# Kernel tuning notes

Hardware: AMD Instinct MI355X
Metric: run time of the kernel (lower is better)

Reference implementation:

```python
import jax, jax.numpy as jnp
import numpy as np

B, T, V, D, OUT = 32, 100, 10000, 128, 1000
CODE_P = 0.003  # ~30 active codes per visit


def gru_dir(x3, whh, bhh, reverse):
    """x3: [B,T,3F] precomputed input-side gates (W_ih x + b_ih). PyTorch GRU math."""
    F = whh.shape[1]
    h0 = jnp.zeros((x3.shape[0], F), x3.dtype)

    def step(h, xt):
        gh = h @ whh.T + bhh
        xr, xz, xn = jnp.split(xt, 3, -1)
        hr, hz, hn = jnp.split(gh, 3, -1)
        r = jax.nn.sigmoid(xr + hr)
        z = jax.nn.sigmoid(xz + hz)
        n = jnp.tanh(xn + r * hn)
        h_new = (1.0 - z) * n + z * h
        return h_new, h_new

    _, hs = jax.lax.scan(step, h0, jnp.swapaxes(x3, 0, 1), reverse=reverse)
    return jnp.swapaxes(hs, 0, 1)  # [B,T,F]


def setup_inputs() -> dict:
    key = jax.random.key(0)
    ks = jax.random.split(key, 16)
    s = lambda k, *sh: jax.random.normal(k, sh, dtype=jnp.float32) * 0.05
    # multi-hot visits, ~0/1 with density CODE_P; force code 0 present so no all-zero visit
    x = (jax.random.uniform(ks[0], (B, T, V)) < CODE_P).astype(jnp.float32)
    x = x.at[:, :, 0].set(1.0)
    return {
        "batchdata": x,
        "emb": s(ks[1], V, D),
        "wih_f": s(ks[2], 3 * D, D), "whh_f": s(ks[3], 3 * D, D),
        "bih_f": jnp.zeros((3 * D,), jnp.float32), "bhh_f": jnp.zeros((3 * D,), jnp.float32),
        "wih_b": s(ks[4], 3 * D, D), "whh_b": s(ks[5], 3 * D, D),
        "bih_b": jnp.zeros((3 * D,), jnp.float32), "bhh_b": jnp.zeros((3 * D,), jnp.float32),
        "attn_w": s(ks[6], 2 * D, 1), "attn_b": jnp.zeros((1,), jnp.float32),
        "comb_w": s(ks[7], D, 4 * D), "comb_b": jnp.zeros((D,), jnp.float32),
        "fc_w": s(ks[8], OUT, D), "fc_b": jnp.zeros((OUT,), jnp.float32),
    }


def reference(batchdata, emb, wih_f, whh_f, bih_f, bhh_f, wih_b, whh_b, bih_b, bhh_b,
              attn_w, attn_b, comb_w, comb_b, fc_w, fc_b):
    # multihot_to_embedding: sum of embedding rows where visit==1 == multihot @ table
    e = jnp.einsum('btv,vd->btd', batchdata, emb)          # [B,T,D]
    mask = jnp.any(e != 0, axis=2)                          # [B,T]
    # DipoleLayer: bidirectional GRU (hidden=D each dir), dropout in eval mode = identity
    xf = jnp.einsum('btf,gf->btg', e, wih_f) + bih_f
    xb = jnp.einsum('btf,gf->btg', e, wih_b) + bih_b
    hf = gru_dir(xf, whh_f, bhh_f, reverse=False)
    hb = gru_dir(xb, whh_b, bhh_b, reverse=True)
    h = jnp.concatenate([hf, hb], axis=-1)                  # [B,T,2D]
    # location-based attention over timesteps
    scores = (h @ attn_w)[..., 0] + attn_b[0]               # [B,T]
    scores = jnp.where(mask, scores, jnp.float32(-1e9))
    a = jax.nn.softmax(scores, axis=-1)
    c = jnp.einsum('bt,btf->bf', a, h)                      # [B,2D] context
    last = jnp.sum(mask.astype(jnp.int32), axis=-1) - 1     # last valid visit
    h_last = h[jnp.arange(h.shape[0]), last]                # [B,2D]
    feat = jnp.tanh(jnp.concatenate([c, h_last], -1) @ comb_w.T + comb_b)  # [B,D]
    logits = feat @ fc_w.T + fc_b                           # [B,OUT]
    return logits
```

## Files before the change

### kernel.cpp

```cpp
#include <hip/hip_runtime.h>
#include <math.h>

#define BB 32
#define TT 100
#define VV 10000
#define DD 128
#define OUTN 1000
#define G3 384

__global__ __launch_bounds__(256) void k_embed(
    const float* __restrict__ x, const float* __restrict__ emb,
    float* __restrict__ e, int* __restrict__ mask)
{
    const int bt  = blockIdx.x;
    const int tid = threadIdx.x;
    __shared__ int   s_cnt;
    __shared__ int   s_any;
    __shared__ int   s_idx[256];
    __shared__ float s_val[256];
    if (tid == 0) { s_cnt = 0; s_any = 0; }
    __syncthreads();

    const float4* x4 = (const float4*)(x + (size_t)bt * VV);
    for (int i = tid; i < VV / 4; i += 256) {
        float4 v = x4[i];
        if (v.x != 0.f) { int p = atomicAdd(&s_cnt, 1); if (p < 256) { s_idx[p] = 4*i+0; s_val[p] = v.x; } }
        if (v.y != 0.f) { int p = atomicAdd(&s_cnt, 1); if (p < 256) { s_idx[p] = 4*i+1; s_val[p] = v.y; } }
        if (v.z != 0.f) { int p = atomicAdd(&s_cnt, 1); if (p < 256) { s_idx[p] = 4*i+2; s_val[p] = v.z; } }
        if (v.w != 0.f) { int p = atomicAdd(&s_cnt, 1); if (p < 256) { s_idx[p] = 4*i+3; s_val[p] = v.w; } }
    }
    __syncthreads();
    int cnt = s_cnt; if (cnt > 256) cnt = 256;
    if (tid < DD) {
        float a0 = 0.f, a1 = 0.f, a2 = 0.f, a3 = 0.f;
        int i = 0;
        for (; i + 4 <= cnt; i += 4) {
            a0 += s_val[i+0] * emb[(size_t)s_idx[i+0] * DD + tid];
            a1 += s_val[i+1] * emb[(size_t)s_idx[i+1] * DD + tid];
            a2 += s_val[i+2] * emb[(size_t)s_idx[i+2] * DD + tid];
            a3 += s_val[i+3] * emb[(size_t)s_idx[i+3] * DD + tid];
        }
        for (; i < cnt; ++i)
            a0 += s_val[i] * emb[(size_t)s_idx[i] * DD + tid];
        float acc = (a0 + a1) + (a2 + a3);
        e[(size_t)bt * DD + tid] = acc;
        if (acc != 0.f) s_any = 1;
    }
    __syncthreads();
    if (tid == 0) mask[bt] = s_any;
}

__global__ __launch_bounds__(256) void k_gates(
    const float* __restrict__ e,
    const float* __restrict__ wih_f, const float* __restrict__ bih_f,
    const float* __restrict__ wih_b, const float* __restrict__ bih_b,
    float* __restrict__ x3)
{
    const int r0  = blockIdx.x * 8;
    const int tid = threadIdx.x;
    __shared__ __align__(16) float se[8][DD];
    for (int i = tid; i < 8 * DD; i += 256)
        se[i >> 7][i & 127] = e[(size_t)(r0 + (i >> 7)) * DD + (i & 127)];
    __syncthreads();

    const float4* wp[3];
    float bias[3];
    #pragma unroll
    for (int cc = 0; cc < 3; ++cc) {
        int col = tid + cc * 256;
        if (col < G3) { wp[cc] = (const float4*)(wih_f + (size_t)col * DD);        bias[cc] = bih_f[col]; }
        else          { wp[cc] = (const float4*)(wih_b + (size_t)(col - G3) * DD); bias[cc] = bih_b[col - G3]; }
    }

    float acc[3][8];
    #pragma unroll
    for (int cc = 0; cc < 3; ++cc)
        #pragma unroll
        for (int r = 0; r < 8; ++r) acc[cc][r] = 0.f;

    for (int k4 = 0; k4 < DD / 4; ++k4) {
        float4 ev[8];
        #pragma unroll
        for (int r = 0; r < 8; ++r) ev[r] = *(const float4*)&se[r][4 * k4];
        #pragma unroll
        for (int cc = 0; cc < 3; ++cc) {
            float4 w = wp[cc][k4];
            #pragma unroll
            for (int r = 0; r < 8; ++r)
                acc[cc][r] += ev[r].x * w.x + ev[r].y * w.y + ev[r].z * w.z + ev[r].w * w.w;
        }
    }
    #pragma unroll
    for (int cc = 0; cc < 3; ++cc) {
        int col = tid + cc * 256;
        #pragma unroll
        for (int r = 0; r < 8; ++r)
            x3[(size_t)(r0 + r) * 768 + col] = acc[cc][r] + bias[cc];
    }
}

__global__ __launch_bounds__(384, 1) void k_gru(
    const float* __restrict__ x3,
    const float* __restrict__ whh_f, const float* __restrict__ bhh_f,
    const float* __restrict__ whh_b, const float* __restrict__ bhh_b,
    float* __restrict__ h_all)
{
    const int dir = blockIdx.x & 1;
    const int b   = blockIdx.x >> 1;
    const int tid = threadIdx.x;
    const int s   = tid & 3;
    const int rg  = tid >> 2;
    const float* whh = dir ? whh_b : whh_f;
    const float* bhh = dir ? bhh_b : bhh_f;

    float4 w4[4][8];
    float  bh[4];
    #pragma unroll
    for (int j = 0; j < 4; ++j) {
        const float4* wr = (const float4*)(whh + (size_t)(rg * 4 + j) * DD + s * 32);
        #pragma unroll
        for (int k4 = 0; k4 < 8; ++k4) w4[j][k4] = wr[k4];
        bh[j] = (s == 0) ? bhh[rg * 4 + j] : 0.f;
    }

    __shared__ __align__(16) float h_pad[4 * 36];
    __shared__ float gh[G3];
    __shared__ __align__(16) float h_hist[TT * DD];

    float h_reg = 0.f;
    if (tid < 144) h_pad[tid] = 0.f;

    const int g = tid;
    const size_t xbase = (size_t)b * TT * 768 + (size_t)dir * G3;
    float xr = 0.f, xz = 0.f, xn = 0.f;
    if (tid < DD) {
        const float* xp = x3 + xbase + (size_t)(dir ? TT - 1 : 0) * 768;
        xr = xp[g]; xz = xp[DD + g]; xn = xp[2 * DD + g];
    }
    __syncthreads();

    for (int t = 0; t < TT; ++t) {
        float nxr = 0.f, nxz = 0.f, nxn = 0.f;
        if (tid < DD && t + 1 < TT) {
            const float* xp = x3 + xbase + (size_t)(dir ? TT - 2 - t : t + 1) * 768;
            nxr = xp[g]; nxz = xp[DD + g]; nxn = xp[2 * DD + g];
        }

        float a0 = bh[0], a1 = bh[1], a2 = bh[2], a3 = bh[3];
        #pragma unroll
        for (int k4 = 0; k4 < 8; ++k4) {
            float4 hv = *(const float4*)&h_pad[s * 36 + 4 * k4];
            a0 += w4[0][k4].x * hv.x + w4[0][k4].y * hv.y + w4[0][k4].z * hv.z + w4[0][k4].w * hv.w;
            a1 += w4[1][k4].x * hv.x + w4[1][k4].y * hv.y + w4[1][k4].z * hv.z + w4[1][k4].w * hv.w;
            a2 += w4[2][k4].x * hv.x + w4[2][k4].y * hv.y + w4[2][k4].z * hv.z + w4[2][k4].w * hv.w;
            a3 += w4[3][k4].x * hv.x + w4[3][k4].y * hv.y + w4[3][k4].z * hv.z + w4[3][k4].w * hv.w;
        }
        a0 += __shfl_xor(a0, 1); a1 += __shfl_xor(a1, 1);
        a2 += __shfl_xor(a2, 1); a3 += __shfl_xor(a3, 1);
        a0 += __shfl_xor(a0, 2); a1 += __shfl_xor(a1, 2);
        a2 += __shfl_xor(a2, 2); a3 += __shfl_xor(a3, 2);
        float my = (s == 0) ? a0 : (s == 1) ? a1 : (s == 2) ? a2 : a3;
        gh[tid] = my;
        __syncthreads();

        if (tid < DD) {
            float hr = gh[g], hz = gh[DD + g], hn = gh[2 * DD + g];
            float r = 1.f / (1.f + __expf(-(xr + hr)));
            float z = 1.f / (1.f + __expf(-(xz + hz)));
            float narg = xn + r * hn;
            float et = __expf(-2.f * fabsf(narg));
            float n = (1.f - et) / (1.f + et);
            n = narg >= 0.f ? n : -n;
            float hnew = (1.f - z) * n + z * h_reg;
            h_reg = hnew;
            h_pad[(g >> 5) * 36 + (g & 31)] = hnew;
            h_hist[(dir ? TT - 1 - t : t) * DD + g] = hnew;
        }
        xr = nxr; xz = nxz; xn = nxn;
        __syncthreads();
    }

    float4* dst = (float4*)(h_all + (size_t)(dir * BB + b) * TT * DD);
    const float4* src = (const float4*)h_hist;
    for (int i = tid; i < TT * DD / 4; i += 384) dst[i] = src[i];
}

__global__ __launch_bounds__(256) void k_attn(
    const float* __restrict__ h_all, const int* __restrict__ mask,
    const float* __restrict__ attn_w, const float* __restrict__ attn_b,
    const float* __restrict__ comb_w, const float* __restrict__ comb_b,
    const float* __restrict__ fc_w, const float* __restrict__ fc_b,
    float* __restrict__ out)
{
    const int b   = blockIdx.x;
    const int tid = threadIdx.x;
    __shared__ float s_aw[256];
    __shared__ float s_sc[128];
    __shared__ int   s_m[128];
    __shared__ float s_red[128];
    __shared__ __align__(16) float s_ch[512];
    __shared__ __align__(16) float s_feat[DD];

    s_aw[tid] = attn_w[tid];
    int m = 0;
    if (tid < 128) {
        m = (tid < TT) ? mask[b * TT + tid] : 0;
        s_m[tid] = m;
    }
    __syncthreads();
    for (int s = 64; s > 0; s >>= 1) {
        if (tid < s) s_m[tid] += s_m[tid + s];
        __syncthreads();
    }
    const int last = s_m[0] - 1;

    const float* hf = h_all + (size_t)(0 * BB + b) * TT * DD;
    const float* hb = h_all + (size_t)(1 * BB + b) * TT * DD;

    float sc = -1e9f;
    if (tid < TT) {
        float a = attn_b[0];
        const float4* hf4 = (const float4*)(hf + (size_t)tid * DD);
        const float4* hb4 = (const float4*)(hb + (size_t)tid * DD);
        for (int k = 0; k < DD / 4; ++k) {
            float4 v = hf4[k];
            a += v.x * s_aw[4*k] + v.y * s_aw[4*k+1] + v.z * s_aw[4*k+2] + v.w * s_aw[4*k+3];
        }
        for (int k = 0; k < DD / 4; ++k) {
            float4 v = hb4[k];
            a += v.x * s_aw[DD+4*k] + v.y * s_aw[DD+4*k+1] + v.z * s_aw[DD+4*k+2] + v.w * s_aw[DD+4*k+3];
        }
        sc = m ? a : -1e9f;
    }
    if (tid < 128) { s_sc[tid] = sc; s_red[tid] = sc; }
    __syncthreads();
    for (int s = 64; s > 0; s >>= 1) {
        if (tid < s) s_red[tid] = fmaxf(s_red[tid], s_red[tid + s]);
        __syncthreads();
    }
    const float mx = s_red[0];
    __syncthreads();
    float ex = 0.f;
    if (tid < 128) { ex = __expf(s_sc[tid] - mx); s_sc[tid] = ex; s_red[tid] = ex; }
    __syncthreads();
    for (int s = 64; s > 0; s >>= 1) {
        if (tid < s) s_red[tid] += s_red[tid + s];
        __syncthreads();
    }
    const float inv = 1.f / s_red[0];
    __syncthreads();

    {
        const int fl = tid & 127;
        const float* hp = (tid < 128) ? hf : hb;
        float csum = 0.f;
        for (int t = 0; t < TT; ++t)
            csum += s_sc[t] * hp[(size_t)t * DD + fl];
        s_ch[tid]       = csum * inv;
        s_ch[256 + tid] = hp[(size_t)last * DD + fl];
    }
    __syncthreads();

    if (tid < 128) {
        float a = comb_b[tid];
        const float4* cw = (const float4*)(comb_w + (size_t)tid * 512);
        for (int k = 0; k < 128; ++k) {
            float4 w4 = cw[k];
            float4 v4 = *(const float4*)&s_ch[4 * k];
            a += w4.x * v4.x + w4.y * v4.y + w4.z * v4.z + w4.w * v4.w;
        }
        s_feat[tid] = tanhf(a);
    }
    __syncthreads();

    for (int o = tid; o < OUTN; o += 256) {
        float a0 = 0.f, a1 = 0.f;
        const float4* w4 = (const float4*)(fc_w + (size_t)o * DD);
        #pragma unroll
        for (int k = 0; k < DD / 8; ++k) {
            float4 w_0 = w4[2*k],   v_0 = *(const float4*)&s_feat[8*k];
            float4 w_1 = w4[2*k+1], v_1 = *(const float4*)&s_feat[8*k+4];
            a0 += w_0.x * v_0.x + w_0.y * v_0.y + w_0.z * v_0.z + w_0.w * v_0.w;
            a1 += w_1.x * v_1.x + w_1.y * v_1.y + w_1.z * v_1.z + w_1.w * v_1.w;
        }
        out[(size_t)b * OUTN + o] = a0 + a1 + fc_b[o];
    }
}

extern "C" void kernel_launch(void* const* d_in, const int* in_sizes, int n_in,
                              void* d_out, int out_size, void* d_ws, size_t ws_size,
                              hipStream_t stream)
{
    const float* x      = (const float*)d_in[0];
    const float* emb    = (const float*)d_in[1];
    const float* wih_f  = (const float*)d_in[2];
    const float* whh_f  = (const float*)d_in[3];
    const float* bih_f  = (const float*)d_in[4];
    const float* bhh_f  = (const float*)d_in[5];
    const float* wih_b  = (const float*)d_in[6];
    const float* whh_b  = (const float*)d_in[7];
    const float* bih_b  = (const float*)d_in[8];
    const float* bhh_b  = (const float*)d_in[9];
    const float* attn_w = (const float*)d_in[10];
    const float* attn_b = (const float*)d_in[11];
    const float* comb_w = (const float*)d_in[12];
    const float* comb_b = (const float*)d_in[13];
    const float* fc_w   = (const float*)d_in[14];
    const float* fc_b   = (const float*)d_in[15];
    float* out = (float*)d_out;

    float* ws    = (float*)d_ws;
    float* e     = ws;
    int*   mask  = (int*)(ws + 409600);
    float* x3    = ws + 412800;
    float* h_all = ws + 2870400;

    k_embed <<<BB * TT,      256, 0, stream>>>(x, emb, e, mask);
    k_gates <<<(BB * TT)/8,  256, 0, stream>>>(e, wih_f, bih_f, wih_b, bih_b, x3);
    k_gru   <<<2 * BB,       384, 0, stream>>>(x3, whh_f, bhh_f, whh_b, bhh_b, h_all);
    k_attn  <<<BB,           256, 0, stream>>>(h_all, mask, attn_w, attn_b,
                                               comb_w, comb_b, fc_w, fc_b, out);
}
```

Baseline: 410.0 us.

## Restructure GRU step to one barrier, batch embed loads, stage attention in LDS

```diff
diff --git a/kernel.cpp b/kernel.cpp
--- a/kernel.cpp
+++ b/kernel.cpp
@@ -22,12 +22,21 @@
     __syncthreads();
 
     const float4* x4 = (const float4*)(x + (size_t)bt * VV);
-    for (int i = tid; i < VV / 4; i += 256) {
-        float4 v = x4[i];
-        if (v.x != 0.f) { int p = atomicAdd(&s_cnt, 1); if (p < 256) { s_idx[p] = 4*i+0; s_val[p] = v.x; } }
-        if (v.y != 0.f) { int p = atomicAdd(&s_cnt, 1); if (p < 256) { s_idx[p] = 4*i+1; s_val[p] = v.y; } }
-        if (v.z != 0.f) { int p = atomicAdd(&s_cnt, 1); if (p < 256) { s_idx[p] = 4*i+2; s_val[p] = v.z; } }
-        if (v.w != 0.f) { int p = atomicAdd(&s_cnt, 1); if (p < 256) { s_idx[p] = 4*i+3; s_val[p] = v.w; } }
+    float4 v[10];
+    #pragma unroll
+    for (int k = 0; k < 10; ++k) {
+        int i = tid + k * 256;
+        int ic = i < 2500 ? i : 2499;
+        v[k] = x4[ic];
+        if (i >= 2500) { v[k].x = 0.f; v[k].y = 0.f; v[k].z = 0.f; v[k].w = 0.f; }
+    }
+    #pragma unroll
+    for (int k = 0; k < 10; ++k) {
+        int base = (tid + k * 256) * 4;
+        if (v[k].x != 0.f) { int p = atomicAdd(&s_cnt, 1); if (p < 256) { s_idx[p] = base+0; s_val[p] = v[k].x; } }
+        if (v[k].y != 0.f) { int p = atomicAdd(&s_cnt, 1); if (p < 256) { s_idx[p] = base+1; s_val[p] = v[k].y; } }
+        if (v[k].z != 0.f) { int p = atomicAdd(&s_cnt, 1); if (p < 256) { s_idx[p] = base+2; s_val[p] = v[k].z; } }
+        if (v[k].w != 0.f) { int p = atomicAdd(&s_cnt, 1); if (p < 256) { s_idx[p] = base+3; s_val[p] = v[k].w; } }
     }
     __syncthreads();
     int cnt = s_cnt; if (cnt > 256) cnt = 256;
@@ -99,7 +108,7 @@
     }
 }
 
-__global__ __launch_bounds__(384, 1) void k_gru(
+__global__ __launch_bounds__(512, 2) void k_gru(
     const float* __restrict__ x3,
     const float* __restrict__ whh_f, const float* __restrict__ bhh_f,
     const float* __restrict__ whh_b, const float* __restrict__ bhh_b,
@@ -109,71 +118,62 @@
     const int b   = blockIdx.x >> 1;
     const int tid = threadIdx.x;
     const int s   = tid & 3;
-    const int rg  = tid >> 2;
+    const int g   = tid >> 2;
     const float* whh = dir ? whh_b : whh_f;
     const float* bhh = dir ? bhh_b : bhh_f;
 
-    float4 w4[4][8];
-    float  bh[4];
-    #pragma unroll
-    for (int j = 0; j < 4; ++j) {
-        const float4* wr = (const float4*)(whh + (size_t)(rg * 4 + j) * DD + s * 32);
-        #pragma unroll
-        for (int k4 = 0; k4 < 8; ++k4) w4[j][k4] = wr[k4];
-        bh[j] = (s == 0) ? bhh[rg * 4 + j] : 0.f;
-    }
-
-    __shared__ __align__(16) float h_pad[4 * 36];
-    __shared__ float gh[G3];
+    float4 wr[8], wz[8], wn[8];
+    {
+        const float4* p0 = (const float4*)(whh + (size_t)(g      ) * DD + s * 32);
+        const float4* p1 = (const float4*)(whh + (size_t)(g + 128) * DD + s * 32);
+        const float4* p2 = (const float4*)(whh + (size_t)(g + 256) * DD + s * 32);
+        #pragma unroll
+        for (int k = 0; k < 8; ++k) { wr[k] = p0[k]; wz[k] = p1[k]; wn[k] = p2[k]; }
+    }
+    const float br = bhh[g], bz = bhh[g + 128], bn = bhh[g + 256];
+
+    __shared__ __align__(16) float h_buf[2][144];
     __shared__ __align__(16) float h_hist[TT * DD];
-
+    if (tid < 144) h_buf[0][tid] = 0.f;
+
+    const size_t xrow = (size_t)b * TT * 768 + (size_t)dir * G3;
+    {
+        const float* xp = x3 + xrow + (size_t)(dir ? TT - 1 : 0) * 768;
+    }
+    const float* xp0 = x3 + xrow + (size_t)(dir ? TT - 1 : 0) * 768;
+    float xr = xp0[g], xz = xp0[DD + g], xn = xp0[2 * DD + g];
     float h_reg = 0.f;
-    if (tid < 144) h_pad[tid] = 0.f;
-
-    const int g = tid;
-    const size_t xbase = (size_t)b * TT * 768 + (size_t)dir * G3;
-    float xr = 0.f, xz = 0.f, xn = 0.f;
-    if (tid < DD) {
-        const float* xp = x3 + xbase + (size_t)(dir ? TT - 1 : 0) * 768;
-        xr = xp[g]; xz = xp[DD + g]; xn = xp[2 * DD + g];
-    }
     __syncthreads();
 
     for (int t = 0; t < TT; ++t) {
+        const int rb = t & 1, wb = rb ^ 1;
         float nxr = 0.f, nxz = 0.f, nxn = 0.f;
-        if (tid < DD && t + 1 < TT) {
-            const float* xp = x3 + xbase + (size_t)(dir ? TT - 2 - t : t + 1) * 768;
-            nxr = xp[g]; nxz = xp[DD + g]; nxn = xp[2 * DD + g];
-        }
-
-        float a0 = bh[0], a1 = bh[1], a2 = bh[2], a3 = bh[3];
-        #pragma unroll
-        for (int k4 = 0; k4 < 8; ++k4) {
-            float4 hv = *(const float4*)&h_pad[s * 36 + 4 * k4];
-            a0 += w4[0][k4].x * hv.x + w4[0][k4].y * hv.y + w4[0][k4].z * hv.z + w4[0][k4].w * hv.w;
-            a1 += w4[1][k4].x * hv.x + w4[1][k4].y * hv.y + w4[1][k4].z * hv.z + w4[1][k4].w * hv.w;
-            a2 += w4[2][k4].x * hv.x + w4[2][k4].y * hv.y + w4[2][k4].z * hv.z + w4[2][k4].w * hv.w;
-            a3 += w4[3][k4].x * hv.x + w4[3][k4].y * hv.y + w4[3][k4].z * hv.z + w4[3][k4].w * hv.w;
-        }
-        a0 += __shfl_xor(a0, 1); a1 += __shfl_xor(a1, 1);
-        a2 += __shfl_xor(a2, 1); a3 += __shfl_xor(a3, 1);
-        a0 += __shfl_xor(a0, 2); a1 += __shfl_xor(a1, 2);
-        a2 += __shfl_xor(a2, 2); a3 += __shfl_xor(a3, 2);
-        float my = (s == 0) ? a0 : (s == 1) ? a1 : (s == 2) ? a2 : a3;
-        gh[tid] = my;
-        __syncthreads();
-
-        if (tid < DD) {
-            float hr = gh[g], hz = gh[DD + g], hn = gh[2 * DD + g];
-            float r = 1.f / (1.f + __expf(-(xr + hr)));
-            float z = 1.f / (1.f + __expf(-(xz + hz)));
-            float narg = xn + r * hn;
-            float et = __expf(-2.f * fabsf(narg));
-            float n = (1.f - et) / (1.f + et);
-            n = narg >= 0.f ? n : -n;
-            float hnew = (1.f - z) * n + z * h_reg;
-            h_reg = hnew;
-            h_pad[(g >> 5) * 36 + (g & 31)] = hnew;
+        if (t + 1 < TT) {
+            const float* np = x3 + xrow + (size_t)(dir ? TT - 2 - t : t + 1) * 768;
+            nxr = np[g]; nxz = np[DD + g]; nxn = np[2 * DD + g];
+        }
+
+        float ar = 0.f, az = 0.f, an = 0.f;
+        #pragma unroll
+        for (int k = 0; k < 8; ++k) {
+            float4 hv = *(const float4*)&h_buf[rb][s * 36 + 4 * k];
+            ar += wr[k].x * hv.x + wr[k].y * hv.y + wr[k].z * hv.z + wr[k].w * hv.w;
+            az += wz[k].x * hv.x + wz[k].y * hv.y + wz[k].z * hv.z + wz[k].w * hv.w;
+            an += wn[k].x * hv.x + wn[k].y * hv.y + wn[k].z * hv.z + wn[k].w * hv.w;
+        }
+        ar += __shfl_xor(ar, 1); az += __shfl_xor(az, 1); an += __shfl_xor(an, 1);
+        ar += __shfl_xor(ar, 2); az += __shfl_xor(az, 2); an += __shfl_xor(an, 2);
+
+        float r    = 1.f / (1.f + __expf(-(xr + ar + br)));
+        float z    = 1.f / (1.f + __expf(-(xz + az + bz)));
+        float narg = xn + r * (an + bn);
+        float et   = __expf(-2.f * fabsf(narg));
+        float n    = (1.f - et) / (1.f + et);
+        n = narg >= 0.f ? n : -n;
+        float hnew = (1.f - z) * n + z * h_reg;
+        h_reg = hnew;
+        if (s == 0) {
+            h_buf[wb][(g >> 5) * 36 + (g & 31)] = hnew;
             h_hist[(dir ? TT - 1 - t : t) * DD + g] = hnew;
         }
         xr = nxr; xz = nxz; xn = nxn;
@@ -182,7 +182,7 @@
 
     float4* dst = (float4*)(h_all + (size_t)(dir * BB + b) * TT * DD);
     const float4* src = (const float4*)h_hist;
-    for (int i = tid; i < TT * DD / 4; i += 384) dst[i] = src[i];
+    for (int i = tid; i < TT * DD / 4; i += 512) dst[i] = src[i];
 }
 
 __global__ __launch_bounds__(256) void k_attn(
@@ -194,6 +194,7 @@
 {
     const int b   = blockIdx.x;
     const int tid = threadIdx.x;
+    __shared__ __align__(16) float s_h[TT * 256];
     __shared__ float s_aw[256];
     __shared__ float s_sc[128];
     __shared__ int   s_m[128];
@@ -201,6 +202,17 @@
     __shared__ __align__(16) float s_ch[512];
     __shared__ __align__(16) float s_feat[DD];
 
+    const float* hf = h_all + (size_t)(0 * BB + b) * TT * DD;
+    const float* hb = h_all + (size_t)(1 * BB + b) * TT * DD;
+    {
+        const float4* hf4 = (const float4*)hf;
+        const float4* hb4 = (const float4*)hb;
+        for (int i = tid; i < TT * DD / 4; i += 256) {
+            int t = i >> 5, c = i & 31;
+            *(float4*)&s_h[t * 256 +       c * 4] = hf4[i];
+            *(float4*)&s_h[t * 256 + 128 + c * 4] = hb4[i];
+        }
+    }
     s_aw[tid] = attn_w[tid];
     int m = 0;
     if (tid < 128) {
@@ -213,9 +225,6 @@
         __syncthreads();
     }
     const int last = s_m[0] - 1;
-
-    const float* hf = h_all + (size_t)(0 * BB + b) * TT * DD;
-    const float* hb = h_all + (size_t)(1 * BB + b) * TT * DD;
 
     float sc = -1e9f;
     if (tid < TT) {
@@ -251,19 +260,24 @@
     __syncthreads();
 
     {
-        const int fl = tid & 127;
-        const float* hp = (tid < 128) ? hf : hb;
-        float csum = 0.f;
-        for (int t = 0; t < TT; ++t)
-            csum += s_sc[t] * hp[(size_t)t * DD + fl];
-        s_ch[tid]       = csum * inv;
-        s_ch[256 + tid] = hp[(size_t)last * DD + fl];
+        float c0 = 0.f, c1 = 0.f, c2 = 0.f, c3 = 0.f;
+        int t = 0;
+        for (; t + 4 <= TT; t += 4) {
+            c0 += s_sc[t+0] * s_h[(t+0) * 256 + tid];
+            c1 += s_sc[t+1] * s_h[(t+1) * 256 + tid];
+            c2 += s_sc[t+2] * s_h[(t+2) * 256 + tid];
+            c3 += s_sc[t+3] * s_h[(t+3) * 256 + tid];
+        }
+        for (; t < TT; ++t) c0 += s_sc[t] * s_h[t * 256 + tid];
+        s_ch[tid]       = ((c0 + c1) + (c2 + c3)) * inv;
+        s_ch[256 + tid] = s_h[last * 256 + tid];
     }
     __syncthreads();
 
     if (tid < 128) {
         float a = comb_b[tid];
         const float4* cw = (const float4*)(comb_w + (size_t)tid * 512);
+        #pragma unroll 4
         for (int k = 0; k < 128; ++k) {
             float4 w4 = cw[k];
             float4 v4 = *(const float4*)&s_ch[4 * k];
@@ -317,7 +331,7 @@
 
     k_embed <<<BB * TT,      256, 0, stream>>>(x, emb, e, mask);
     k_gates <<<(BB * TT)/8,  256, 0, stream>>>(e, wih_f, bih_f, wih_b, bih_b, x3);
-    k_gru   <<<2 * BB,       384, 0, stream>>>(x3, whh_f, bhh_f, whh_b, bhh_b, h_all);
+    k_gru   <<<2 * BB,       512, 0, stream>>>(x3, whh_f, bhh_f, whh_b, bhh_b, h_all);
     k_attn  <<<BB,           256, 0, stream>>>(h_all, mask, attn_w, attn_b,
                                                comb_w, comb_b, fc_w, fc_b, out);
 }
```

Result: no change. 409.0 us (-0.2%).
